# Performance work log

Hardware: AMD Instinct MI355X
Metric: run time of the kernel (lower is better)

The kernel has to match this reference:

```python
import jax, jax.numpy as jnp
import numpy as np

N = 100000   # nodes
D = 64       # in_features == out_features
E = 1600000  # edges (avg degree 16)
C = 1.0      # curvature
MIN_NORM = 1e-15
PROJ_EPS = 1e-5
ATANH_CLIP = 1.0 - 1e-7


def _artanh(x):
    return jnp.arctanh(jnp.clip(x, -ATANH_CLIP, ATANH_CLIP))


def _norm(x):
    return jnp.clip(jnp.linalg.norm(x, axis=-1, keepdims=True), MIN_NORM)


def setup_inputs() -> dict:
    key = jax.random.key(0)
    k1, k2, k3, k4, k5 = jax.random.split(key, 5)
    # points inside the unit ball (module assumes input already on manifold)
    x = 0.05 * jax.random.normal(k1, (N, D), dtype=jnp.float32)
    # xavier_uniform with gain sqrt(2): std ~= sqrt(2)*sqrt(2/(D+D))
    W = jax.random.normal(k2, (D, D), dtype=jnp.float32) * np.float32(np.sqrt(4.0 / (2 * D)))
    edge_vals = jax.random.uniform(k3, (E,), dtype=jnp.float32) / 16.0  # ~normalized adjacency
    rows = jax.random.randint(k4, (E,), 0, N, dtype=jnp.int32)
    cols = jax.random.randint(k5, (E,), 0, N, dtype=jnp.int32)
    return {"x": x, "W": W, "edge_vals": edge_vals, "rows": rows, "cols": cols}


def reference(x, W, edge_vals, rows, cols):
    sc = jnp.sqrt(jnp.float32(C))
    # --- Poincare Linear: mobius_matvec(W, x, c) (no bias, eval-mode dropout) ---
    mx = x @ W.T                                  # [N, D]
    x_n = _norm(x)
    mx_n = _norm(mx)
    res = jnp.tanh(mx_n / x_n * _artanh(sc * x_n)) * mx / (mx_n * sc)
    res = jnp.where(jnp.all(mx == 0, axis=-1, keepdims=True), 0.0, res)
    # --- poincare2euclidean == logmap0 ---
    p_n = _norm(res)
    hidden = _artanh(sc * p_n) * res / (sc * p_n)  # tangent at origin
    # --- sparse adjacency matmul: support = adj @ hidden ---
    gathered = edge_vals[:, None] * hidden[cols]   # [E, D]
    support = jax.ops.segment_sum(gathered, rows, num_segments=N)
    # --- euclidean2poincare == expmap0 ---
    u_n = _norm(support)
    p = jnp.tanh(sc * u_n) * support / (sc * u_n)
    # --- Act: relu(logmap0) -> proj_tan0 (identity) -> expmap0 -> proj ---
    pn2 = _norm(p)
    xt = jax.nn.relu(_artanh(sc * pn2) * p / (sc * pn2))
    xt_n = _norm(xt)
    out = jnp.tanh(sc * xt_n) * xt / (sc * xt_n)
    o_n = _norm(out)
    max_n = (1.0 - PROJ_EPS) / sc
    out = jnp.where(o_n > max_n, out / o_n * max_n, out)
    return out
```

## Files before the change

### kernel.cpp

```cpp
#include <hip/hip_runtime.h>
#include <hip/hip_fp16.h>

#define NN 100000
#define DD 64
#define EE 1600000
#define NB 512
#define NPB 196
#define CHUNK 3125
#define CAP 3520

typedef _Float16 half8 __attribute__((ext_vector_type(8)));
typedef float floatx4 __attribute__((ext_vector_type(4)));

__device__ __forceinline__ float frcp(float x) { return __builtin_amdgcn_rcpf(x); }

__device__ __forceinline__ float fast_tanh(float x) {
    float t = __expf(2.0f * x);
    return (t - 1.0f) * frcp(t + 1.0f);
}
__device__ __forceinline__ float fast_atanh(float x) {
    const float CLIP = 1.0f - 1e-7f;
    x = fminf(fmaxf(x, -CLIP), CLIP);
    return 0.5f * __logf((1.0f + x) * frcp(1.0f - x));
}
__device__ __forceinline__ float group16_reduce_sum(float v) {
    #pragma unroll
    for (int m = 8; m > 0; m >>= 1) v += __shfl_xor(v, m, 16);
    return v;
}
__device__ __forceinline__ float lo16f(unsigned u) {
    return __half2float(__ushort_as_half((unsigned short)(u & 0xFFFFu)));
}
__device__ __forceinline__ float hi16f(unsigned u) {
    return __half2float(__ushort_as_half((unsigned short)(u >> 16)));
}

__global__ __launch_bounds__(1024) void linear_count_kernel(
    const float* __restrict__ x, const float* __restrict__ W,
    const int* __restrict__ rows,
    __half* __restrict__ hidden, int* __restrict__ cnt) {
    __shared__ _Float16 Wh[64 * 80];
    __shared__ int h[NB];
    const int t = threadIdx.x;

    if (t < NB) h[t] = 0;
    for (int i = t; i < 64 * 64; i += 1024)
        Wh[(i >> 6) * 80 + (i & 63)] = (_Float16)W[i];
    __syncthreads();

    {
        const int e0 = blockIdx.x * CHUNK;
        for (int i = t; i < CHUNK; i += 1024)
            atomicAdd(&h[(unsigned)rows[e0 + i] / NPB], 1);
    }

    const int lane = t & 63;
    const int wv   = t >> 6;
    if (wv < 13) {
        const int q    = lane >> 4;
        const int c    = lane & 15;
        const int node = blockIdx.x * NPB + wv * 16 + c;
        const int node_ld = (node < NN) ? node : (NN - 1);

        const float MIN_NORM = 1e-15f;
        const float4* xr = (const float4*)(x + node_ld * 64);
        float4 b0a = xr[q * 2];
        float4 b0b = xr[q * 2 + 1];
        float4 b1a = xr[8 + q * 2];
        float4 b1b = xr[8 + q * 2 + 1];

        float xpart = b0a.x*b0a.x + b0a.y*b0a.y + b0a.z*b0a.z + b0a.w*b0a.w
                    + b0b.x*b0b.x + b0b.y*b0b.y + b0b.z*b0b.z + b0b.w*b0b.w
                    + b1a.x*b1a.x + b1a.y*b1a.y + b1a.z*b1a.z + b1a.w*b1a.w
                    + b1b.x*b1b.x + b1b.y*b1b.y + b1b.z*b1b.z + b1b.w*b1b.w;
        xpart += __shfl_xor(xpart, 16, 64);
        xpart += __shfl_xor(xpart, 32, 64);
        float x_n = fmaxf(sqrtf(xpart), MIN_NORM);

        half8 bf0, bf1;
        bf0[0]=(_Float16)b0a.x; bf0[1]=(_Float16)b0a.y; bf0[2]=(_Float16)b0a.z; bf0[3]=(_Float16)b0a.w;
        bf0[4]=(_Float16)b0b.x; bf0[5]=(_Float16)b0b.y; bf0[6]=(_Float16)b0b.z; bf0[7]=(_Float16)b0b.w;
        bf1[0]=(_Float16)b1a.x; bf1[1]=(_Float16)b1a.y; bf1[2]=(_Float16)b1a.z; bf1[3]=(_Float16)b1a.w;
        bf1[4]=(_Float16)b1b.x; bf1[5]=(_Float16)b1b.y; bf1[6]=(_Float16)b1b.z; bf1[7]=(_Float16)b1b.w;

        floatx4 acc[4];
        #pragma unroll
        for (int tt = 0; tt < 4; ++tt) {
            const half8* a0 = (const half8*)&Wh[(16 * tt + c) * 80 + q * 8];
            const half8* a1 = (const half8*)&Wh[(16 * tt + c) * 80 + 32 + q * 8];
            floatx4 z = {0.f, 0.f, 0.f, 0.f};
            z = __builtin_amdgcn_mfma_f32_16x16x32_f16(a0[0], bf0, z, 0, 0, 0);
            z = __builtin_amdgcn_mfma_f32_16x16x32_f16(a1[0], bf1, z, 0, 0, 0);
            acc[tt] = z;
        }

        float hscale = fast_atanh(x_n) * frcp(x_n);

        if (node < NN) {
            #pragma unroll
            for (int tt = 0; tt < 4; ++tt) {
                __half2 lo = __floats2half2_rn(acc[tt][0] * hscale, acc[tt][1] * hscale);
                __half2 hi = __floats2half2_rn(acc[tt][2] * hscale, acc[tt][3] * hscale);
                uint2 pkt;
                pkt.x = *(unsigned*)&lo;
                pkt.y = *(unsigned*)&hi;
                ((uint2*)hidden)[node * 16 + tt * 4 + q] = pkt;
            }
        }
    }
    __syncthreads();
    if (t < NB) cnt[blockIdx.x * NB + t] = h[t];
}

__global__ __launch_bounds__(512) void offset_kernel(const int* __restrict__ cnt,
                                                     int* __restrict__ woff,
                                                     int* __restrict__ gcount) {
    const int lane = threadIdx.x & 63;
    const int b    = blockIdx.x * 8 + (threadIdx.x >> 6);
    int c[8]; int sum = 0;
    #pragma unroll
    for (int k = 0; k < 8; ++k) { c[k] = cnt[(lane * 8 + k) * NB + b]; sum += c[k]; }
    int pre = sum;
    #pragma unroll
    for (int m = 1; m < 64; m <<= 1) {
        int u = __shfl_up(pre, m, 64);
        if (lane >= m) pre += u;
    }
    int run = pre - sum;
    #pragma unroll
    for (int k = 0; k < 8; ++k) { woff[(lane * 8 + k) * NB + b] = run; run += c[k]; }
    if (lane == 63) gcount[b] = run;
}

__global__ __launch_bounds__(64) void scan_kernel(const int* __restrict__ gcount,
                                                  int* __restrict__ bbase) {
    const int lane = threadIdx.x;
    int c[8]; int sum = 0;
    #pragma unroll
    for (int k = 0; k < 8; ++k) { c[k] = gcount[lane * 8 + k]; sum += c[k]; }
    int pre = sum;
    #pragma unroll
    for (int m = 1; m < 64; m <<= 1) {
        int u = __shfl_up(pre, m, 64);
        if (lane >= m) pre += u;
    }
    int run = pre - sum;
    #pragma unroll
    for (int k = 0; k < 8; ++k) { bbase[lane * 8 + k] = run; run += c[k]; }
    if (lane == 63) bbase[NB] = run;
}

__global__ __launch_bounds__(1024) void sort_scatter_kernel(
    const int* __restrict__ rows, const int* __restrict__ cols,
    const float* __restrict__ ev, const int* __restrict__ cnt,
    const int* __restrict__ woff, const int* __restrict__ bbase,
    int* __restrict__ csr_desc, __half* __restrict__ csr_val) {
    __shared__ int cur[NB];
    __shared__ int delta[NB];
    __shared__ int sdesc[CHUNK];
    __shared__ __half sval[CHUNK];
    __shared__ unsigned short bid[CHUNK];
    const int t  = threadIdx.x;
    const int e0 = blockIdx.x * CHUNK;

    if (t < 64) {
        const int lane = t;
        int c[8]; int sum = 0;
        #pragma unroll
        for (int k = 0; k < 8; ++k) { c[k] = cnt[blockIdx.x * NB + lane * 8 + k]; sum += c[k]; }
        int pre = sum;
        #pragma unroll
        for (int m = 1; m < 64; m <<= 1) {
            int u = __shfl_up(pre, m, 64);
            if (lane >= m) pre += u;
        }
        int run = pre - sum;
        #pragma unroll
        for (int k = 0; k < 8; ++k) {
            int b = lane * 8 + k;
            cur[b]   = run;
            delta[b] = bbase[b] + woff[blockIdx.x * NB + b] - run;
            run += c[k];
        }
    }
    __syncthreads();
    for (int i = t; i < CHUNK; i += 1024) {
        unsigned r = (unsigned)rows[e0 + i];
        unsigned c = (unsigned)cols[e0 + i];
        float v = ev[e0 + i];
        unsigned b  = r / NPB;
        unsigned rl = r - b * NPB;
        int idx = atomicAdd(&cur[b], 1);
        sdesc[idx] = (int)((rl << 24) | (c << 7));
        sval[idx]  = __float2half(v);
        bid[idx]   = (unsigned short)b;
    }
    __syncthreads();
    for (int i = t; i < CHUNK; i += 1024) {
        int gpos = delta[bid[i]] + i;
        csr_desc[gpos] = sdesc[i];
        csr_val[gpos]  = sval[i];
    }
}

__global__ __launch_bounds__(1024) void sortgather_kernel(
    const __half* __restrict__ hidden, const int* __restrict__ csr_desc,
    const __half* __restrict__ csr_val, const int* __restrict__ bbase,
    float* __restrict__ out) {
    __shared__ int2 srt[CAP];
    __shared__ int raw_desc[CAP];
    __shared__ __half raw_val[CAP];
    __shared__ int cnt_a[NPB];
    __shared__ int start[NPB];
    __shared__ int cur[NPB];
    const int t  = threadIdx.x;
    const int b  = blockIdx.x;
    const int lo = bbase[b];
    int cnt = bbase[b + 1] - lo;
    if (cnt > CAP) cnt = CAP;

    if (t < NPB) cnt_a[t] = 0;
    __syncthreads();
    for (int i = t; i < cnt; i += 1024) {
        int d = csr_desc[lo + i];
        raw_desc[i] = d;
        raw_val[i]  = csr_val[lo + i];
        atomicAdd(&cnt_a[((unsigned)d) >> 24], 1);
    }
    __syncthreads();
    if (t < 64) {
        const int lane = t;
        int c[4]; int sum = 0;
        #pragma unroll
        for (int k = 0; k < 4; ++k) {
            int bb = lane * 4 + k;
            c[k] = (bb < NPB) ? cnt_a[bb] : 0;
            sum += c[k];
        }
        int pre = sum;
        #pragma unroll
        for (int m = 1; m < 64; m <<= 1) {
            int u = __shfl_up(pre, m, 64);
            if (lane >= m) pre += u;
        }
        int run = pre - sum;
        #pragma unroll
        for (int k = 0; k < 4; ++k) {
            int bb = lane * 4 + k;
            if (bb < NPB) { start[bb] = run; cur[bb] = run; run += c[k]; }
        }
    }
    __syncthreads();
    for (int i = t; i < cnt; i += 1024) {
        int d = raw_desc[i];
        float v = __half2float(raw_val[i]);
        int rl = ((unsigned)d) >> 24;
        int p  = atomicAdd(&cur[rl], 1);
        srt[p] = make_int2(d, __float_as_int(v));
    }
    __syncthreads();

    const int lane = t & 63;
    const int wv   = t >> 6;
    const int g    = lane >> 4;
    const int l8   = (lane & 15) * 8;
    const char* __restrict__ hidc = (const char*)hidden;
    const float MIN_NORM = 1e-15f;
    const float MAX_N = 1.0f - 1e-5f;

    for (int n = wv; n < NPB; n += 16) {
        int i   = start[n];
        int rhi = i + cnt_a[n];
        float ax = 0.f, ay = 0.f, az = 0.f, aw = 0.f;

        for (; i + 8 <= rhi; i += 8) {
            int2 dA = srt[i + g];
            int2 dB = srt[i + 4 + g];
            unsigned oA = (((unsigned)dA.x) & 0xFFFFFFu) + l8;
            unsigned oB = (((unsigned)dB.x) & 0xFFFFFFu) + l8;
            uint2 hA = *(const uint2*)(hidc + oA);
            uint2 hB = *(const uint2*)(hidc + oB);
            float vA = __int_as_float(dA.y);
            float vB = __int_as_float(dB.y);
            ax = fmaf(vA, lo16f(hA.x), ax);
            ay = fmaf(vA, hi16f(hA.x), ay);
            az = fmaf(vA, lo16f(hA.y), az);
            aw = fmaf(vA, hi16f(hA.y), aw);
            ax = fmaf(vB, lo16f(hB.x), ax);
            ay = fmaf(vB, hi16f(hB.x), ay);
            az = fmaf(vB, lo16f(hB.y), az);
            aw = fmaf(vB, hi16f(hB.y), aw);
        }
        for (; i < rhi; i += 4) {
            int idx = i + g;
            int2 d = srt[(idx < rhi) ? idx : (rhi - 1)];
            float v = (idx < rhi) ? __int_as_float(d.y) : 0.0f;
            unsigned o = (((unsigned)d.x) & 0xFFFFFFu) + l8;
            uint2 h = *(const uint2*)(hidc + o);
            ax = fmaf(v, lo16f(h.x), ax);
            ay = fmaf(v, hi16f(h.x), ay);
            az = fmaf(v, lo16f(h.y), az);
            aw = fmaf(v, hi16f(h.y), aw);
        }

        ax += __shfl_xor(ax, 16, 64); ax += __shfl_xor(ax, 32, 64);
        ay += __shfl_xor(ay, 16, 64); ay += __shfl_xor(ay, 32, 64);
        az += __shfl_xor(az, 16, 64); az += __shfl_xor(az, 32, 64);
        aw += __shfl_xor(aw, 16, 64); aw += __shfl_xor(aw, 32, 64);

        float xx = fmaxf(ax, 0.f), xy = fmaxf(ay, 0.f);
        float xz = fmaxf(az, 0.f), xw = fmaxf(aw, 0.f);

        float part = xx*xx + xy*xy + xz*xz + xw*xw;
        float xt_n = fmaxf(sqrtf(group16_reduce_sum(part)), MIN_NORM);
        float txt  = fast_tanh(xt_n);
        float s3   = txt * frcp(xt_n);
        if (txt > MAX_N) s3 = MAX_N * frcp(xt_n);
        float ox = xx*s3, oy = xy*s3, oz = xz*s3, ow = xw*s3;

        int gn = b * NPB + n;
        if (g == 0 && gn < NN) {
            float4 o4 = make_float4(ox, oy, oz, ow);
            *(float4*)(out + gn * DD + (lane & 15) * 4) = o4;
        }
    }
}

extern "C" void kernel_launch(void* const* d_in, const int* in_sizes, int n_in,
                              void* d_out, int out_size, void* d_ws, size_t ws_size,
                              hipStream_t stream) {
    const float* x    = (const float*)d_in[0];
    const float* W    = (const float*)d_in[1];
    const float* ev   = (const float*)d_in[2];
    const int*   rows = (const int*)d_in[3];
    const int*   cols = (const int*)d_in[4];
    float* out = (float*)d_out;

    char* ws = (char*)d_ws;
    __half* hidden   = (__half*)ws;
    int*    csr_desc = (int*)(ws + 12800000);
    __half* csr_val  = (__half*)(ws + 19200000);
    int*    cnt      = (int*)(ws + 22400000);
    int*    woff     = (int*)(ws + 23448576);
    int*    gcount   = (int*)(ws + 24497152);
    int*    bbase    = (int*)(ws + 24499200);

    linear_count_kernel<<<NB, 1024, 0, stream>>>(x, W, rows, hidden, cnt);
    offset_kernel<<<NB / 8, 512, 0, stream>>>(cnt, woff, gcount);
    scan_kernel<<<1, 64, 0, stream>>>(gcount, bbase);
    sort_scatter_kernel<<<NB, 1024, 0, stream>>>(rows, cols, ev, cnt, woff, bbase,
                                                 csr_desc, csr_val);
    sortgather_kernel<<<NB, 1024, 0, stream>>>(hidden, csr_desc, csr_val, bbase, out);
}
```

Measured before the change: 150.6 us.

## Fold global bucket scan into consumer kernels and remap linear-stage node tiling

Removes the single-block scan kernel launch. Each block of the scatter and gather kernels now redundantly computes the 512-entry prefix scan of bucket counts from gcount with one wavefront. The linear stage now maps all 16 waves to 256 nodes per block and runs it only in the first 392 blocks, instead of 13 waves covering 196 nodes in every block. This saves a launch and its serialization gap, at the cost of a small redundant scan per block and less even spread of the linear work.

Result: no change. 153.4 us (+1.8%).

```diff
diff --git a/kernel.cpp b/kernel.cpp
--- a/kernel.cpp
+++ b/kernel.cpp
@@ -8,6 +8,7 @@
 #define NPB 196
 #define CHUNK 3125
 #define CAP 3520
+#define LINB 392
 
 typedef _Float16 half8 __attribute__((ext_vector_type(8)));
 typedef float floatx4 __attribute__((ext_vector_type(4)));
@@ -33,6 +34,22 @@
 }
 __device__ __forceinline__ float hi16f(unsigned u) {
     return __half2float(__ushort_as_half((unsigned short)(u >> 16)));
+}
+
+__device__ __forceinline__ void wave_scan512(const int* __restrict__ gcount,
+                                             int lane, int* base8 ) {
+    int c[8]; int sum = 0;
+    #pragma unroll
+    for (int k = 0; k < 8; ++k) { c[k] = gcount[lane * 8 + k]; sum += c[k]; }
+    int pre = sum;
+    #pragma unroll
+    for (int m = 1; m < 64; m <<= 1) {
+        int u = __shfl_up(pre, m, 64);
+        if (lane >= m) pre += u;
+    }
+    int run = pre - sum;
+    #pragma unroll
+    for (int k = 0; k < 8; ++k) { base8[k] = run; run += c[k]; }
 }
 
 __global__ __launch_bounds__(1024) void linear_count_kernel(
@@ -54,12 +71,12 @@
             atomicAdd(&h[(unsigned)rows[e0 + i] / NPB], 1);
     }
 
-    const int lane = t & 63;
-    const int wv   = t >> 6;
-    if (wv < 13) {
+    if (blockIdx.x < LINB) {
+        const int lane = t & 63;
+        const int wv   = t >> 6;
         const int q    = lane >> 4;
         const int c    = lane & 15;
-        const int node = blockIdx.x * NPB + wv * 16 + c;
+        const int node = blockIdx.x * 256 + wv * 16 + c;
         const int node_ld = (node < NN) ? node : (NN - 1);
 
         const float MIN_NORM = 1e-15f;
@@ -132,28 +149,10 @@
     if (lane == 63) gcount[b] = run;
 }
 
-__global__ __launch_bounds__(64) void scan_kernel(const int* __restrict__ gcount,
-                                                  int* __restrict__ bbase) {
-    const int lane = threadIdx.x;
-    int c[8]; int sum = 0;
-    #pragma unroll
-    for (int k = 0; k < 8; ++k) { c[k] = gcount[lane * 8 + k]; sum += c[k]; }
-    int pre = sum;
-    #pragma unroll
-    for (int m = 1; m < 64; m <<= 1) {
-        int u = __shfl_up(pre, m, 64);
-        if (lane >= m) pre += u;
-    }
-    int run = pre - sum;
-    #pragma unroll
-    for (int k = 0; k < 8; ++k) { bbase[lane * 8 + k] = run; run += c[k]; }
-    if (lane == 63) bbase[NB] = run;
-}
-
 __global__ __launch_bounds__(1024) void sort_scatter_kernel(
     const int* __restrict__ rows, const int* __restrict__ cols,
     const float* __restrict__ ev, const int* __restrict__ cnt,
-    const int* __restrict__ woff, const int* __restrict__ bbase,
+    const int* __restrict__ woff, const int* __restrict__ gcount,
     int* __restrict__ csr_desc, __half* __restrict__ csr_val) {
     __shared__ int cur[NB];
     __shared__ int delta[NB];
@@ -165,6 +164,8 @@
 
     if (t < 64) {
         const int lane = t;
+        int base8[8];
+        wave_scan512(gcount, lane, base8);
         int c[8]; int sum = 0;
         #pragma unroll
         for (int k = 0; k < 8; ++k) { c[k] = cnt[blockIdx.x * NB + lane * 8 + k]; sum += c[k]; }
@@ -179,7 +180,7 @@
         for (int k = 0; k < 8; ++k) {
             int b = lane * 8 + k;
             cur[b]   = run;
-            delta[b] = bbase[b] + woff[blockIdx.x * NB + b] - run;
+            delta[b] = base8[k] + woff[blockIdx.x * NB + b] - run;
             run += c[k];
         }
     }
@@ -205,7 +206,7 @@
 
 __global__ __launch_bounds__(1024) void sortgather_kernel(
     const __half* __restrict__ hidden, const int* __restrict__ csr_desc,
-    const __half* __restrict__ csr_val, const int* __restrict__ bbase,
+    const __half* __restrict__ csr_val, const int* __restrict__ gcount,
     float* __restrict__ out) {
     __shared__ int2 srt[CAP];
     __shared__ int raw_desc[CAP];
@@ -213,14 +214,25 @@
     __shared__ int cnt_a[NPB];
     __shared__ int start[NPB];
     __shared__ int cur[NPB];
+    __shared__ int sh_lo, sh_cnt;
     const int t  = threadIdx.x;
     const int b  = blockIdx.x;
-    const int lo = bbase[b];
-    int cnt = bbase[b + 1] - lo;
+
+    if (t < NPB) cnt_a[t] = 0;
+    if (t < 64) {
+        int base8[8];
+        wave_scan512(gcount, t, base8);
+        #pragma unroll
+        for (int k = 0; k < 8; ++k) {
+            int bb = t * 8 + k;
+            if (bb == b) { sh_lo = base8[k]; sh_cnt = gcount[bb]; }
+        }
+    }
+    __syncthreads();
+    const int lo = sh_lo;
+    int cnt = sh_cnt;
     if (cnt > CAP) cnt = CAP;
 
-    if (t < NPB) cnt_a[t] = 0;
-    __syncthreads();
     for (int i = t; i < cnt; i += 1024) {
         int d = csr_desc[lo + i];
         raw_desc[i] = d;
@@ -343,12 +355,10 @@
     int*    cnt      = (int*)(ws + 22400000);
     int*    woff     = (int*)(ws + 23448576);
     int*    gcount   = (int*)(ws + 24497152);
-    int*    bbase    = (int*)(ws + 24499200);
 
     linear_count_kernel<<<NB, 1024, 0, stream>>>(x, W, rows, hidden, cnt);
     offset_kernel<<<NB / 8, 512, 0, stream>>>(cnt, woff, gcount);
-    scan_kernel<<<1, 64, 0, stream>>>(gcount, bbase);
-    sort_scatter_kernel<<<NB, 1024, 0, stream>>>(rows, cols, ev, cnt, woff, bbase,
+    sort_scatter_kernel<<<NB, 1024, 0, stream>>>(rows, cols, ev, cnt, woff, gcount,
                                                  csr_desc, csr_val);
-    sortgather_kernel<<<NB, 1024, 0, stream>>>(hidden, csr_desc, csr_val, bbase, out);
-}
+    sortgather_kernel<<<NB, 1024, 0, stream>>>(hidden, csr_desc, csr_val, gcount, out);
+}
```
